# Kernel optimization log

Measured on AMD Instinct MI355X. Metric: run time of the kernel, lower is better.

The kernel has to match this reference:

```python
import jax, jax.numpy as jnp
import numpy as np

TWO_PI = 2.0 * np.pi
OMEGA = 1.0  # frequency scale from init


def setup_inputs() -> dict:
    key = jax.random.key(0)
    ks = jax.random.split(key, 10)
    B, G, D = 2, 32, 3
    C_IN, C, C_OUT, F, L = 4, 128, 2, 128, 4  # in/model/out channels, freqs, n_spectral_convs
    a = jax.random.normal(ks[0], (B, G, G, G, C_IN), dtype=jnp.float32)
    x = jax.random.uniform(ks[1], (B, G, G, G, D), dtype=jnp.float32)
    y = jax.random.uniform(ks[2], (B, G, G, G, D), dtype=jnp.float32)
    fc_in_w = jax.random.normal(ks[3], (C_IN, C), dtype=jnp.float32) / np.sqrt(C_IN)
    fc_in_b = jnp.zeros((C,), dtype=jnp.float32)
    freqs = jax.random.normal(ks[4], (L, F, D), dtype=jnp.float32)  # per-layer spatial frequencies
    w_real = jax.random.normal(ks[5], (L, C, C, F), dtype=jnp.float32) * 0.05
    w_imag = jax.random.normal(ks[6], (L, C, C, F), dtype=jnp.float32) * 0.05
    fc_out_w = jax.random.normal(ks[7], (C, C_OUT), dtype=jnp.float32) / np.sqrt(C)
    fc_out_b = jnp.zeros((C_OUT,), dtype=jnp.float32)
    return {"a": a, "x": x, "y": y, "fc_in_w": fc_in_w, "fc_in_b": fc_in_b,
            "freqs": freqs, "w_real": w_real, "w_imag": w_imag,
            "fc_out_w": fc_out_w, "fc_out_b": fc_out_b}


def _spectral_conv(hf, xin, xout, k, Wc):
    # hf: (B, N, C) real; xin/xout: (B, N, D); k: (F, D); Wc: (C, C, F) complex
    N = hf.shape[1]
    ang_in = TWO_PI * OMEGA * jnp.einsum('bnd,fd->bnf', xin, k)
    phi_in = jnp.exp(-1j * ang_in.astype(jnp.complex64))          # (B, N, F)
    H = jnp.einsum('bnc,bnf->bcf', hf.astype(jnp.complex64), phi_in) / N  # forward transform
    G = jnp.einsum('bcf,cof->bof', H, Wc)                          # per-frequency channel mixing
    ang_out = TWO_PI * OMEGA * jnp.einsum('bnd,fd->bnf', xout, k)
    phi_out = jnp.exp(1j * ang_out.astype(jnp.complex64))          # (B, N, F)
    return jnp.real(jnp.einsum('bof,bnf->bno', G, phi_out))       # inverse evaluation at xout


def reference(a, x, y, fc_in_w, fc_in_b, freqs, w_real, w_imag, fc_out_w, fc_out_b):
    B = a.shape[0]
    spatial = a.shape[1:4]
    hf = jnp.einsum('...i,io->...o', a, fc_in_w) + fc_in_b
    hf = hf.reshape(B, -1, hf.shape[-1])               # (B, N, C)
    xf = x.reshape(B, -1, x.shape[-1])                 # (B, N, D)
    yf = y.reshape(B, -1, y.shape[-1])
    L = freqs.shape[0]
    for l in range(L):
        Wc = (w_real[l] + 1j * w_imag[l]).astype(jnp.complex64)
        pts_out = xf if l < L - 1 else yf              # last conv queries at y
        hf = jax.nn.gelu(_spectral_conv(hf, xf, pts_out, freqs[l], Wc))
    u = jnp.einsum('bnc,co->bno', hf, fc_out_w) + fc_out_b
    return u.reshape(B, *spatial, fc_out_w.shape[-1])
```

## Files before the change

kernel.cpp:

```cpp
#include <hip/hip_runtime.h>
#include <math.h>

#define Bb 2
#define Nn 32768
#define Cc 128
#define Ff 128
#define LL 4
#define SKN 128
#define PS 16448

typedef __attribute__((ext_vector_type(8))) short short8;
typedef __attribute__((ext_vector_type(4))) float float4v;
typedef __attribute__((ext_vector_type(2))) unsigned int uint2v;
typedef unsigned short ushort_t;
typedef unsigned int uint_t;

union frag_cast { short8 s; uint_t u[4]; };
union vec8 { float4v v[2]; float s[8]; };

__device__ inline uint_t asu(float f) { union { float f; uint_t u; } x; x.f = f; return x.u; }
__device__ inline float asf(uint_t u) { union { uint_t u; float f; } x; x.u = u; return x.f; }
__device__ inline uint_t pack_hi(float v0, float v1) {
    return __builtin_amdgcn_perm(asu(v1), asu(v0), 0x07060302u);
}
__device__ inline float resid(float v) { return v - asf(asu(v) & 0xffff0000u); }

typedef __attribute__((address_space(1))) const uint_t guint;
typedef __attribute__((address_space(3))) uint_t luint;
__device__ inline void gload16(const uint_t* g, uint_t* l) {
    __builtin_amdgcn_global_load_lds((guint*)g, (luint*)l, 16, 0, 0);
}

#define LBAR() asm volatile("s_waitcnt lgkmcnt(0)\n\ts_barrier" ::: "memory")
#define CBAR() asm volatile("s_waitcnt vmcnt(6) lgkmcnt(0)\n\ts_barrier" ::: "memory")

__global__ __launch_bounds__(256) void prep_xt(const float* __restrict__ x,
                                               const float* __restrict__ y,
                                               float* __restrict__ xT,
                                               float* __restrict__ yT) {
    int i = blockIdx.x * 256 + threadIdx.x;
    int b = i >> 15, n = i & 32767;
    const float* xp = x + (size_t)i * 3;
    const float* yp = y + (size_t)i * 3;
    size_t base = ((size_t)(b * 3) << 15) + n;
    xT[base] = xp[0]; xT[base + (1 << 15)] = xp[1]; xT[base + (2 << 15)] = xp[2];
    yT[base] = yp[0]; yT[base + (1 << 15)] = yp[1]; yT[base + (2 << 15)] = yp[2];
}

__global__ __launch_bounds__(256) void in_proj(const float* __restrict__ a,
                                               const float* __restrict__ w,
                                               const float* __restrict__ bias,
                                               uint_t* __restrict__ hfTh,
                                               uint_t* __restrict__ hfTl) {
    int idx = blockIdx.x * 256 + threadIdx.x;
    int np = idx & 16383;
    int c = (idx >> 14) & 127;
    int b = idx >> 21;
    int n = np * 2;
    const float* ap = a + (((size_t)(b << 15)) + n) * 4;
    float s0 = bias[c], s1 = s0;
#pragma unroll
    for (int i = 0; i < 4; ++i) { s0 += ap[i] * w[i * Cc + c]; s1 += ap[4 + i] * w[i * Cc + c]; }
    hfTh[idx] = pack_hi(s0, s1);
    hfTl[idx] = pack_hi(resid(s0), resid(s1));
}

__global__ __launch_bounds__(512, 2) void fwd_lds(const uint_t* __restrict__ hfTh,
                                                  const uint_t* __restrict__ hfTl,
                                                  const float* __restrict__ xT,
                                                  const float* __restrict__ freqs,
                                                  float* __restrict__ Spart) {
    __shared__ __align__(16) uint_t Ah_s[2][2048], Al_s[2][2048];

    const int sk = blockIdx.x;
    const int b = blockIdx.y;
    const int tid = threadIdx.x, lane = tid & 63, wave = tid >> 6;
    const int h = wave & 1, wn = wave >> 1;
    const int fr = lane & 15, kg = lane >> 4;

    float kx[2], ky[2], kz[2];
#pragma unroll
    for (int ni = 0; ni < 2; ++ni) {
        int f = wn * 32 + ni * 16 + fr;
        kx[ni] = freqs[f * 3 + 0];
        ky[ni] = freqs[f * 3 + 1];
        kz[ni] = freqs[f * 3 + 2];
    }

    const float* xb = xT + ((size_t)(b * 3) << 15);
    const int srow = wave * 16 + (lane >> 2);
    const size_t gbase = ((size_t)(b * 128 + srow) << 14) + (size_t)((lane & 3) * 4);
    const int npair0 = sk * 128;

    float4v acc[8][2];
#pragma unroll
    for (int mi = 0; mi < 8; ++mi)
#pragma unroll
        for (int ni = 0; ni < 2; ++ni) acc[mi][ni] = (float4v){0.f, 0.f, 0.f, 0.f};

    vec8 X0[2], X1[2], X2[2];
    gload16(hfTh + gbase + npair0, &Ah_s[0][wave * 256]);
    gload16(hfTl + gbase + npair0, &Al_s[0][wave * 256]);
    __builtin_amdgcn_sched_barrier(0);
    {
        const int nbase = sk * 256 + kg * 8;
        X0[0].v[0] = *(const float4v*)(xb + nbase);
        X0[0].v[1] = *(const float4v*)(xb + nbase + 4);
        X1[0].v[0] = *(const float4v*)(xb + (1 << 15) + nbase);
        X1[0].v[1] = *(const float4v*)(xb + (1 << 15) + nbase + 4);
        X2[0].v[0] = *(const float4v*)(xb + (2 << 15) + nbase);
        X2[0].v[1] = *(const float4v*)(xb + (2 << 15) + nbase + 4);
    }

#pragma unroll
    for (int kt = 0; kt < 8; ++kt) {
        const int cur = kt & 1, nxt = cur ^ 1;
        CBAR();
        if (kt < 7) {
            gload16(hfTh + gbase + npair0 + (kt + 1) * 16, &Ah_s[nxt][wave * 256]);
            gload16(hfTl + gbase + npair0 + (kt + 1) * 16, &Al_s[nxt][wave * 256]);
            __builtin_amdgcn_sched_barrier(0);
            const int nbase2 = sk * 256 + (kt + 1) * 32 + kg * 8;
            X0[nxt].v[0] = *(const float4v*)(xb + nbase2);
            X0[nxt].v[1] = *(const float4v*)(xb + nbase2 + 4);
            X1[nxt].v[0] = *(const float4v*)(xb + (1 << 15) + nbase2);
            X1[nxt].v[1] = *(const float4v*)(xb + (1 << 15) + nbase2 + 4);
            X2[nxt].v[0] = *(const float4v*)(xb + (2 << 15) + nbase2);
            X2[nxt].v[1] = *(const float4v*)(xb + (2 << 15) + nbase2 + 4);
        }
        float r[16], tv[16];
#pragma unroll
        for (int ni = 0; ni < 2; ++ni)
#pragma unroll
            for (int q = 0; q < 4; ++q) {
                float rv0 = X0[cur].s[2 * q] * kx[ni] + X1[cur].s[2 * q] * ky[ni] + X2[cur].s[2 * q] * kz[ni];
                float rv1 = X0[cur].s[2 * q + 1] * kx[ni] + X1[cur].s[2 * q + 1] * ky[ni] + X2[cur].s[2 * q + 1] * kz[ni];
                r[ni * 8 + 2 * q] = __builtin_amdgcn_fractf(rv0);
                r[ni * 8 + 2 * q + 1] = __builtin_amdgcn_fractf(rv1);
            }
        if (h) {
#pragma unroll
            for (int i = 0; i < 16; ++i) tv[i] = __builtin_amdgcn_sinf(r[i]);
        } else {
#pragma unroll
            for (int i = 0; i < 16; ++i) tv[i] = __builtin_amdgcn_cosf(r[i]);
        }
        frag_cast bhf[2], blf[2];
#pragma unroll
        for (int ni = 0; ni < 2; ++ni)
#pragma unroll
            for (int q = 0; q < 4; ++q) {
                float v0 = tv[ni * 8 + 2 * q], v1 = tv[ni * 8 + 2 * q + 1];
                bhf[ni].u[q] = pack_hi(v0, v1);
                blf[ni].u[q] = pack_hi(resid(v0), resid(v1));
            }
#pragma unroll
        for (int mi = 0; mi < 8; ++mi) {
            frag_cast ah, al;
            ah.s = *(const short8*)&Ah_s[cur][(mi * 16 + fr) * 16 + kg * 4];
            al.s = *(const short8*)&Al_s[cur][(mi * 16 + fr) * 16 + kg * 4];
#pragma unroll
            for (int ni = 0; ni < 2; ++ni) {
                acc[mi][ni] = __builtin_amdgcn_mfma_f32_16x16x32_bf16(ah.s, bhf[ni].s, acc[mi][ni], 0, 0, 0);
                acc[mi][ni] = __builtin_amdgcn_mfma_f32_16x16x32_bf16(ah.s, blf[ni].s, acc[mi][ni], 0, 0, 0);
                acc[mi][ni] = __builtin_amdgcn_mfma_f32_16x16x32_bf16(al.s, bhf[ni].s, acc[mi][ni], 0, 0, 0);
            }
        }
    }

    float* op = Spart + (size_t)((b * 2 + h) * SKN + sk) * PS;
#pragma unroll
    for (int mi = 0; mi < 8; ++mi)
#pragma unroll
        for (int ni = 0; ni < 2; ++ni)
#pragma unroll
            for (int r2 = 0; r2 < 4; ++r2) {
                int c = mi * 16 + kg * 4 + r2;
                int f = wn * 32 + ni * 16 + fr;
                op[c * 128 + f] = acc[mi][ni][r2];
            }
}

__global__ __launch_bounds__(512, 2) void inv_fwd(const uint_t* __restrict__ Gh,
                                                  const uint_t* __restrict__ Gl,
                                                  const float* __restrict__ xT,
                                                  const float* __restrict__ fI,
                                                  const float* __restrict__ fF,
                                                  float* __restrict__ Spart) {
    __shared__ float kxs[128], kys[128], kzs[128];
    __shared__ __align__(16) float Xs[3][256];
    __shared__ __align__(16) uint_t Ah_s[4096], Al_s[4096];
    __shared__ __align__(16) uint_t Hh_s[2560], Hl_s[2560];
    const int chunk = blockIdx.x, b = blockIdx.y;
    const int tid = threadIdx.x, lane = tid & 63, wn = tid >> 6;
    const int fr = lane & 15, kg = lane >> 4;
    const int h = wn & 1, wf = wn >> 1;
    const int n0 = chunk * 256;

    if (tid < 128) {
        kxs[tid] = fI[tid * 3 + 0];
        kys[tid] = fI[tid * 3 + 1];
        kzs[tid] = fI[tid * 3 + 2];
    }
    for (int i = tid; i < 768; i += 512) {
        int d = i >> 8, nn = i & 255;
        Xs[d][nn] = xT[((size_t)(b * 3 + d) << 15) + n0 + nn];
    }

    frag_cast bh[8], bl[8];
#pragma unroll
    for (int kt = 0; kt < 8; ++kt) {
        size_t gi = ((size_t)(b * 128 + wn * 16 + fr)) * 128 + kt * 16 + kg * 4;
        bh[kt].s = *(const short8*)(Gh + gi);
        bl[kt].s = *(const short8*)(Gl + gi);
    }

    float kxf[2], kyf[2], kzf[2];
#pragma unroll
    for (int ni = 0; ni < 2; ++ni) {
        int f = wf * 32 + ni * 16 + fr;
        kxf[ni] = fF[f * 3 + 0];
        kyf[ni] = fF[f * 3 + 1];
        kzf[ni] = fF[f * 3 + 2];
    }

    float4v accF[8][2];
#pragma unroll
    for (int mi = 0; mi < 8; ++mi)
#pragma unroll
        for (int ni = 0; ni < 2; ++ni) accF[mi][ni] = (float4v){0.f, 0.f, 0.f, 0.f};

    __syncthreads();

    for (int p = 0; p < 8; ++p) {
        const int nsub = p * 32;

        {
            const int kt = wn;
            float4v kxv = *(const float4v*)&kxs[kt * 16 + kg * 4];
            float4v kyv = *(const float4v*)&kys[kt * 16 + kg * 4];
            float4v kzv = *(const float4v*)&kzs[kt * 16 + kg * 4];
#pragma unroll
            for (int mi2 = 0; mi2 < 2; ++mi2) {
                float px = Xs[0][nsub + mi2 * 16 + fr];
                float py = Xs[1][nsub + mi2 * 16 + fr];
                float pz = Xs[2][nsub + mi2 * 16 + fr];
                frag_cast ah, al;
#pragma unroll
                for (int q = 0; q < 4; ++q) {
                    float rev = px * kxv[q] + py * kyv[q] + pz * kzv[q];
                    float rr = __builtin_amdgcn_fractf(rev);
                    float cv = __builtin_amdgcn_cosf(rr);
                    float sv = __builtin_amdgcn_sinf(rr);
                    ah.u[q] = pack_hi(cv, sv);
                    al.u[q] = pack_hi(resid(cv), resid(sv));
                }
                *(short8*)&Ah_s[((mi2 * 8 + kt) * 64 + lane) * 4] = ah.s;
                *(short8*)&Al_s[((mi2 * 8 + kt) * 64 + lane) * 4] = al.s;
            }
        }
        LBAR();

        {
            float4v ahh[2], ahl[2], alh[2];
#pragma unroll
            for (int mi2 = 0; mi2 < 2; ++mi2) {
                ahh[mi2] = (float4v){0.f, 0.f, 0.f, 0.f};
                ahl[mi2] = (float4v){0.f, 0.f, 0.f, 0.f};
                alh[mi2] = (float4v){0.f, 0.f, 0.f, 0.f};
            }
#pragma unroll
            for (int kt = 0; kt < 8; ++kt) {
#pragma unroll
                for (int mi2 = 0; mi2 < 2; ++mi2) {
                    frag_cast ah, al;
                    ah.s = *(const short8*)&Ah_s[((mi2 * 8 + kt) * 64 + lane) * 4];
                    al.s = *(const short8*)&Al_s[((mi2 * 8 + kt) * 64 + lane) * 4];
                    ahh[mi2] = __builtin_amdgcn_mfma_f32_16x16x32_bf16(ah.s, bh[kt].s, ahh[mi2], 0, 0, 0);
                    ahl[mi2] = __builtin_amdgcn_mfma_f32_16x16x32_bf16(ah.s, bl[kt].s, ahl[mi2], 0, 0, 0);
                    alh[mi2] = __builtin_amdgcn_mfma_f32_16x16x32_bf16(al.s, bh[kt].s, alh[mi2], 0, 0, 0);
                }
            }
#pragma unroll
            for (int mi2 = 0; mi2 < 2; ++mi2) {
                float g[4];
#pragma unroll
                for (int r2 = 0; r2 < 4; ++r2) {
                    float v = ahh[mi2][r2] + (ahl[mi2][r2] + alh[mi2][r2]);
                    float u2 = 1.5957691216057308f * (v + 0.044715f * v * v * v);
                    float t = 1.0f - 2.0f / (1.0f + __expf(u2));
                    g[r2] = 0.5f * v * (1.0f + t);
                }
                int row = wn * 16 + fr;
                uint2v hv = { pack_hi(g[0], g[1]), pack_hi(g[2], g[3]) };
                uint2v lv = { pack_hi(resid(g[0]), resid(g[1])), pack_hi(resid(g[2]), resid(g[3])) };
                *(uint2v*)&Hh_s[row * 20 + mi2 * 8 + kg * 2] = hv;
                *(uint2v*)&Hl_s[row * 20 + mi2 * 8 + kg * 2] = lv;
            }
        }
        LBAR();

        {
            vec8 x0, x1, x2;
            x0.v[0] = *(const float4v*)&Xs[0][nsub + kg * 8];
            x0.v[1] = *(const float4v*)&Xs[0][nsub + kg * 8 + 4];
            x1.v[0] = *(const float4v*)&Xs[1][nsub + kg * 8];
            x1.v[1] = *(const float4v*)&Xs[1][nsub + kg * 8 + 4];
            x2.v[0] = *(const float4v*)&Xs[2][nsub + kg * 8];
            x2.v[1] = *(const float4v*)&Xs[2][nsub + kg * 8 + 4];
            float r[16], tv[16];
#pragma unroll
            for (int ni = 0; ni < 2; ++ni)
#pragma unroll
                for (int q = 0; q < 4; ++q) {
                    float rv0 = x0.s[2 * q] * kxf[ni] + x1.s[2 * q] * kyf[ni] + x2.s[2 * q] * kzf[ni];
                    float rv1 = x0.s[2 * q + 1] * kxf[ni] + x1.s[2 * q + 1] * kyf[ni] + x2.s[2 * q + 1] * kzf[ni];
                    r[ni * 8 + 2 * q] = __builtin_amdgcn_fractf(rv0);
                    r[ni * 8 + 2 * q + 1] = __builtin_amdgcn_fractf(rv1);
                }
            if (h) {
#pragma unroll
                for (int i = 0; i < 16; ++i) tv[i] = __builtin_amdgcn_sinf(r[i]);
            } else {
#pragma unroll
                for (int i = 0; i < 16; ++i) tv[i] = __builtin_amdgcn_cosf(r[i]);
            }
            frag_cast bhf[2], blf[2];
#pragma unroll
            for (int ni = 0; ni < 2; ++ni)
#pragma unroll
                for (int q = 0; q < 4; ++q) {
                    float v0 = tv[ni * 8 + 2 * q], v1 = tv[ni * 8 + 2 * q + 1];
                    bhf[ni].u[q] = pack_hi(v0, v1);
                    blf[ni].u[q] = pack_hi(resid(v0), resid(v1));
                }
#pragma unroll
            for (int mi = 0; mi < 8; ++mi) {
                frag_cast ah, al;
                ah.s = *(const short8*)&Hh_s[(mi * 16 + fr) * 20 + kg * 4];
                al.s = *(const short8*)&Hl_s[(mi * 16 + fr) * 20 + kg * 4];
#pragma unroll
                for (int ni = 0; ni < 2; ++ni) {
                    accF[mi][ni] = __builtin_amdgcn_mfma_f32_16x16x32_bf16(ah.s, bhf[ni].s, accF[mi][ni], 0, 0, 0);
                    accF[mi][ni] = __builtin_amdgcn_mfma_f32_16x16x32_bf16(ah.s, blf[ni].s, accF[mi][ni], 0, 0, 0);
                    accF[mi][ni] = __builtin_amdgcn_mfma_f32_16x16x32_bf16(al.s, bhf[ni].s, accF[mi][ni], 0, 0, 0);
                }
            }
        }
        LBAR();
    }

    float* op = Spart + (size_t)((b * 2 + h) * SKN + chunk) * PS;
#pragma unroll
    for (int mi = 0; mi < 8; ++mi)
#pragma unroll
        for (int ni = 0; ni < 2; ++ni)
#pragma unroll
            for (int r2 = 0; r2 < 4; ++r2) {
                int c = mi * 16 + kg * 4 + r2;
                int f = wf * 32 + ni * 16 + fr;
                op[c * 128 + f] = accF[mi][ni][r2];
            }
}

__global__ __launch_bounds__(256) void reduce_kernel(const float* __restrict__ Spart,
                                                     float* __restrict__ S) {
    __shared__ float red[4][64];
    const int chunk = blockIdx.x, bh = blockIdx.y;
    const int tid = threadIdx.x;
    const int cfl = tid & 63, q = tid >> 6;
    const float* p = Spart + (size_t)bh * SKN * PS + (size_t)(q * 32) * PS + chunk * 64 + cfl;
    float s = 0.0f;
#pragma unroll 8
    for (int k = 0; k < 32; ++k) s += p[(size_t)k * PS];
    red[q][cfl] = s;
    __syncthreads();
    if (tid < 64) {
        float t = red[0][tid] + red[1][tid] + red[2][tid] + red[3][tid];
        S[bh * 16384 + chunk * 64 + tid] = t;
    }
}

__global__ __launch_bounds__(256) void mix_kernel(const float* __restrict__ S,
                                                  const float* __restrict__ Wre,
                                                  const float* __restrict__ Wim,
                                                  uint_t* __restrict__ Gh,
                                                  uint_t* __restrict__ Gl) {
    __shared__ float Stile[4][128][16];
    const int ot = blockIdx.x;
    const int ft = blockIdx.y;
    const int tid = threadIdx.x;
    const int fl = tid & 15, ol = (tid >> 4) & 1, cg = tid >> 5;
    const int o = ot * 2 + ol, f0 = ft * 16;

    for (int i = tid; i < 8192; i += 256) {
        int bh = i >> 11, c = (i >> 4) & 127, ff = i & 15;
        Stile[bh][c][ff] = S[(size_t)bh * 16384 + c * 128 + f0 + ff];
    }
    __syncthreads();

    float g0 = 0.f, g1 = 0.f, g2 = 0.f, g3 = 0.f;
#pragma unroll 4
    for (int c = cg * 16; c < cg * 16 + 16; ++c) {
        float wr = Wre[((size_t)(c * 128 + o)) * 128 + f0 + fl];
        float wi = Wim[((size_t)(c * 128 + o)) * 128 + f0 + fl];
        float sc0 = Stile[0][c][fl], ss0 = Stile[1][c][fl];
        float sc1 = Stile[2][c][fl], ss1 = Stile[3][c][fl];
        g0 += sc0 * wr + ss0 * wi;  g1 += ss0 * wr - sc0 * wi;
        g2 += sc1 * wr + ss1 * wi;  g3 += ss1 * wr - sc1 * wi;
    }
    __syncthreads();
    float4v* rp = (float4v*)Stile;
    rp[cg * 32 + ol * 16 + fl] = (float4v){g0, g1, g2, g3};
    __syncthreads();
    if (tid < 32) {
        int tol = tid >> 4, tfl = tid & 15;
        float4v r = rp[tid];
#pragma unroll
        for (int j = 1; j < 8; ++j) r += rp[j * 32 + tid];
        const float invN = 1.0f / (float)Nn;
        float gre0 = r[0] * invN, gmi0 = r[1] * invN;
        float gre1 = r[2] * invN, gmi1 = r[3] * invN;
        int oo = ot * 2 + tol;
        Gh[(0 * 128 + oo) * 128 + f0 + tfl] = pack_hi(gre0, gmi0);
        Gl[(0 * 128 + oo) * 128 + f0 + tfl] = pack_hi(resid(gre0), resid(gmi0));
        Gh[(1 * 128 + oo) * 128 + f0 + tfl] = pack_hi(gre1, gmi1);
        Gl[(1 * 128 + oo) * 128 + f0 + tfl] = pack_hi(resid(gre1), resid(gmi1));
    }
}

template <int LAST>
__global__ __launch_bounds__(512, 4) void inv_reg(const uint_t* __restrict__ Gh,
                                                  const uint_t* __restrict__ Gl,
                                                  const float* __restrict__ ptsT,
                                                  const float* __restrict__ freqs,
                                                  uint_t* __restrict__ hfTh,
                                                  uint_t* __restrict__ hfTl,
                                                  const float* __restrict__ ow,
                                                  const float* __restrict__ ob,
                                                  float* __restrict__ u) {
    __shared__ __align__(16) float kxs[128], kys[128], kzs[128];
    __shared__ __align__(16) uint_t Ah_s[4096];
    __shared__ __align__(16) uint_t Al_s[4096];
    __shared__ float redo[8][32][2];
    const int nt = blockIdx.x, b = blockIdx.y;
    const int tid = threadIdx.x, lane = tid & 63, wn = tid >> 6;
    const int fr = lane & 15, kg = lane >> 4;

    if (tid < 128) {
        kxs[tid] = freqs[tid * 3 + 0];
        kys[tid] = freqs[tid * 3 + 1];
        kzs[tid] = freqs[tid * 3 + 2];
    }

    frag_cast bh[8], bl[8];
#pragma unroll
    for (int kt = 0; kt < 8; ++kt) {
        size_t gi = ((size_t)(b * 128 + wn * 16 + fr)) * 128 + kt * 16 + kg * 4;
        bh[kt].s = *(const short8*)(Gh + gi);
        bl[kt].s = *(const short8*)(Gl + gi);
    }

    float w0v = 0.f, w1v = 0.f;
    if (LAST) {
        int o = wn * 16 + fr;
        w0v = ow[o * 2 + 0];
        w1v = ow[o * 2 + 1];
    }

    const float* pb = ptsT + ((size_t)(b * 3) << 15);
    const int n0 = nt * 64;

    float px[4], py[4], pz[4];
#pragma unroll
    for (int m = 0; m < 4; ++m) {
        int n = n0 + m * 16 + fr;
        px[m] = pb[n]; py[m] = pb[(1 << 15) + n]; pz[m] = pb[(2 << 15) + n];
    }

    __syncthreads();

#pragma unroll
    for (int ph = 0; ph < 2; ++ph) {
        {
            const int kt = wn;
            float4v kxv = *(const float4v*)&kxs[kt * 16 + kg * 4];
            float4v kyv = *(const float4v*)&kys[kt * 16 + kg * 4];
            float4v kzv = *(const float4v*)&kzs[kt * 16 + kg * 4];
#pragma unroll
            for (int mi2 = 0; mi2 < 2; ++mi2) {
                const int m = ph * 2 + mi2;
                frag_cast ah, al;
#pragma unroll
                for (int q = 0; q < 4; ++q) {
                    float rev = px[m] * kxv[q] + py[m] * kyv[q] + pz[m] * kzv[q];
                    float rr = __builtin_amdgcn_fractf(rev);
                    float cv = __builtin_amdgcn_cosf(rr);
                    float sv = __builtin_amdgcn_sinf(rr);
                    ah.u[q] = pack_hi(cv, sv);
                    al.u[q] = pack_hi(resid(cv), resid(sv));
                }
                *(short8*)&Ah_s[((mi2 * 8 + kt) * 64 + lane) * 4] = ah.s;
                *(short8*)&Al_s[((mi2 * 8 + kt) * 64 + lane) * 4] = al.s;
            }
        }
        LBAR();

        float4v ahh[2], ahl[2], alh[2];
#pragma unroll
        for (int mi2 = 0; mi2 < 2; ++mi2) {
            ahh[mi2] = (float4v){0.f, 0.f, 0.f, 0.f};
            ahl[mi2] = (float4v){0.f, 0.f, 0.f, 0.f};
            alh[mi2] = (float4v){0.f, 0.f, 0.f, 0.f};
        }
#pragma unroll
        for (int kt = 0; kt < 8; ++kt) {
#pragma unroll
            for (int mi2 = 0; mi2 < 2; ++mi2) {
                frag_cast ah, al;
                ah.s = *(const short8*)&Ah_s[((mi2 * 8 + kt) * 64 + lane) * 4];
                al.s = *(const short8*)&Al_s[((mi2 * 8 + kt) * 64 + lane) * 4];
                ahh[mi2] = __builtin_amdgcn_mfma_f32_16x16x32_bf16(ah.s, bh[kt].s, ahh[mi2], 0, 0, 0);
                ahl[mi2] = __builtin_amdgcn_mfma_f32_16x16x32_bf16(ah.s, bl[kt].s, ahl[mi2], 0, 0, 0);
                alh[mi2] = __builtin_amdgcn_mfma_f32_16x16x32_bf16(al.s, bh[kt].s, alh[mi2], 0, 0, 0);
            }
        }
        LBAR();

        float ps[2][2][4];
        if (LAST) {
#pragma unroll
            for (int mi2 = 0; mi2 < 2; ++mi2)
#pragma unroll
                for (int j = 0; j < 2; ++j)
#pragma unroll
                    for (int r2 = 0; r2 < 4; ++r2) ps[mi2][j][r2] = 0.f;
        }
#pragma unroll
        for (int mi2 = 0; mi2 < 2; ++mi2) {
            const int m = ph * 2 + mi2;
            float g[4];
#pragma unroll
            for (int r2 = 0; r2 < 4; ++r2) {
                float v = ahh[mi2][r2] + (ahl[mi2][r2] + alh[mi2][r2]);
                float u2 = 1.5957691216057308f * (v + 0.044715f * v * v * v);
                float t = 1.0f - 2.0f / (1.0f + __expf(u2));
                g[r2] = 0.5f * v * (1.0f + t);
            }
            if (!LAST) {
                int o = wn * 16 + fr;
                int nb = n0 + m * 16 + kg * 4;
                size_t di = ((size_t)(b * 128 + o) << 14) + (nb >> 1);
                uint2v hv = { pack_hi(g[0], g[1]), pack_hi(g[2], g[3]) };
                uint2v lv = { pack_hi(resid(g[0]), resid(g[1])), pack_hi(resid(g[2]), resid(g[3])) };
                *(uint2v*)(hfTh + di) = hv;
                *(uint2v*)(hfTl + di) = lv;
            } else {
#pragma unroll
                for (int r2 = 0; r2 < 4; ++r2) {
                    ps[mi2][0][r2] += g[r2] * w0v;
                    ps[mi2][1][r2] += g[r2] * w1v;
                }
            }
        }

        if (LAST) {
#pragma unroll
            for (int mi2 = 0; mi2 < 2; ++mi2)
#pragma unroll
                for (int j = 0; j < 2; ++j)
#pragma unroll
                    for (int r2 = 0; r2 < 4; ++r2) {
                        float v = ps[mi2][j][r2];
                        v += __shfl_xor(v, 1);
                        v += __shfl_xor(v, 2);
                        v += __shfl_xor(v, 4);
                        v += __shfl_xor(v, 8);
                        ps[mi2][j][r2] = v;
                    }
            if (fr == 0) {
#pragma unroll
                for (int mi2 = 0; mi2 < 2; ++mi2)
#pragma unroll
                    for (int r2 = 0; r2 < 4; ++r2) {
                        redo[wn][mi2 * 16 + kg * 4 + r2][0] = ps[mi2][0][r2];
                        redo[wn][mi2 * 16 + kg * 4 + r2][1] = ps[mi2][1][r2];
                    }
            }
            LBAR();
            if (tid < 64) {
                int nl = tid >> 1, j = tid & 1;
                float val = ob[j];
#pragma unroll
                for (int w8 = 0; w8 < 8; ++w8) val += redo[w8][nl][j];
                u[((size_t)((b << 15) + n0 + ph * 32 + nl)) * 2 + j] = val;
            }
            LBAR();
        }
    }
}

extern "C" void kernel_launch(void* const* d_in, const int* in_sizes, int n_in,
                              void* d_out, int out_size, void* d_ws, size_t ws_size,
                              hipStream_t stream) {
    const float* a        = (const float*)d_in[0];
    const float* x        = (const float*)d_in[1];
    const float* y        = (const float*)d_in[2];
    const float* fc_in_w  = (const float*)d_in[3];
    const float* fc_in_b  = (const float*)d_in[4];
    const float* freqs    = (const float*)d_in[5];
    const float* w_real   = (const float*)d_in[6];
    const float* w_imag   = (const float*)d_in[7];
    const float* fc_out_w = (const float*)d_in[8];
    const float* fc_out_b = (const float*)d_in[9];
    float* out = (float*)d_out;

    uint_t* ws    = (uint_t*)d_ws;
    uint_t* hfTh  = ws;
    uint_t* hfTl  = hfTh + (size_t)Bb * Cc * Nn / 2;
    float*  Spart = (float*)(hfTl + (size_t)Bb * Cc * Nn / 2);
    float*  S     = Spart + (size_t)Bb * 2 * SKN * PS;
    uint_t* Gh    = (uint_t*)(S + (size_t)Bb * 2 * Cc * Ff);
    uint_t* Gl    = Gh + (size_t)Bb * Cc * Ff;
    float*  xT    = (float*)(Gl + (size_t)Bb * Cc * Ff);
    float*  yT    = xT + (size_t)Bb * 3 * Nn;

    prep_xt<<<(Bb * Nn) / 256, 256, 0, stream>>>(x, y, xT, yT);
    in_proj<<<(Bb * Cc * Nn / 2) / 256, 256, 0, stream>>>(a, fc_in_w, fc_in_b, hfTh, hfTl);

    fwd_lds<<<dim3(SKN, Bb), 512, 0, stream>>>(hfTh, hfTl, xT, freqs, Spart);
    reduce_kernel<<<dim3(256, 4), 256, 0, stream>>>(Spart, S);
    mix_kernel<<<dim3(64, 8), 256, 0, stream>>>(S, w_real, w_imag, Gh, Gl);

    for (int l = 0; l < LL - 1; ++l) {
        const float* kI  = freqs  + (size_t)l * Ff * 3;
        const float* kF  = freqs  + (size_t)(l + 1) * Ff * 3;
        const float* Wre = w_real + (size_t)(l + 1) * Cc * Cc * Ff;
        const float* Wim = w_imag + (size_t)(l + 1) * Cc * Cc * Ff;

        inv_fwd<<<dim3(128, Bb), 512, 0, stream>>>(Gh, Gl, xT, kI, kF, Spart);
        reduce_kernel<<<dim3(256, 4), 256, 0, stream>>>(Spart, S);
        mix_kernel<<<dim3(64, 8), 256, 0, stream>>>(S, Wre, Wim, Gh, Gl);
    }

    inv_reg<1><<<dim3(512, Bb), 512, 0, stream>>>(Gh, Gl, yT, freqs + (size_t)(LL - 1) * Ff * 3,
                                                  hfTh, hfTl, fc_out_w, fc_out_b, out);
}
```

Baseline: 330.7 us.

## Split inv_fwd work across 16 waves per block instead of 8

```diff
diff --git a/kernel.cpp b/kernel.cpp
--- a/kernel.cpp
+++ b/kernel.cpp
@@ -181,20 +181,21 @@
             }
 }
 
-__global__ __launch_bounds__(512, 2) void inv_fwd(const uint_t* __restrict__ Gh,
-                                                  const uint_t* __restrict__ Gl,
-                                                  const float* __restrict__ xT,
-                                                  const float* __restrict__ fI,
-                                                  const float* __restrict__ fF,
-                                                  float* __restrict__ Spart) {
+__global__ __launch_bounds__(1024, 4) void inv_fwd(const uint_t* __restrict__ Gh,
+                                                   const uint_t* __restrict__ Gl,
+                                                   const float* __restrict__ xT,
+                                                   const float* __restrict__ fI,
+                                                   const float* __restrict__ fF,
+                                                   float* __restrict__ Spart) {
     __shared__ float kxs[128], kys[128], kzs[128];
     __shared__ __align__(16) float Xs[3][256];
     __shared__ __align__(16) uint_t Ah_s[4096], Al_s[4096];
     __shared__ __align__(16) uint_t Hh_s[2560], Hl_s[2560];
     const int chunk = blockIdx.x, b = blockIdx.y;
-    const int tid = threadIdx.x, lane = tid & 63, wn = tid >> 6;
+    const int tid = threadIdx.x, lane = tid & 63, wv = tid >> 6;
     const int fr = lane & 15, kg = lane >> 4;
-    const int h = wn & 1, wf = wn >> 1;
+    const int og = wv & 7, mh = wv >> 3;
+    const int h = wv & 1, wf = (wv >> 1) & 3, fh = wv >> 3;
     const int n0 = chunk * 256;
 
     if (tid < 128) {
@@ -202,15 +203,15 @@
         kys[tid] = fI[tid * 3 + 1];
         kzs[tid] = fI[tid * 3 + 2];
     }
-    for (int i = tid; i < 768; i += 512) {
-        int d = i >> 8, nn = i & 255;
+    if (tid < 768) {
+        int d = tid >> 8, nn = tid & 255;
         Xs[d][nn] = xT[((size_t)(b * 3 + d) << 15) + n0 + nn];
     }
 
     frag_cast bh[8], bl[8];
 #pragma unroll
     for (int kt = 0; kt < 8; ++kt) {
-        size_t gi = ((size_t)(b * 128 + wn * 16 + fr)) * 128 + kt * 16 + kg * 4;
+        size_t gi = ((size_t)(b * 128 + og * 16 + fr)) * 128 + kt * 16 + kg * 4;
         bh[kt].s = *(const short8*)(Gh + gi);
         bl[kt].s = *(const short8*)(Gl + gi);
     }
@@ -224,11 +225,11 @@
         kzf[ni] = fF[f * 3 + 2];
     }
 
-    float4v accF[8][2];
-#pragma unroll
-    for (int mi = 0; mi < 8; ++mi)
-#pragma unroll
-        for (int ni = 0; ni < 2; ++ni) accF[mi][ni] = (float4v){0.f, 0.f, 0.f, 0.f};
+    float4v accF[4][2];
+#pragma unroll
+    for (int mi4 = 0; mi4 < 4; ++mi4)
+#pragma unroll
+        for (int ni = 0; ni < 2; ++ni) accF[mi4][ni] = (float4v){0.f, 0.f, 0.f, 0.f};
 
     __syncthreads();
 
@@ -236,67 +237,54 @@
         const int nsub = p * 32;
 
         {
-            const int kt = wn;
+            const int kt = og;
             float4v kxv = *(const float4v*)&kxs[kt * 16 + kg * 4];
             float4v kyv = *(const float4v*)&kys[kt * 16 + kg * 4];
             float4v kzv = *(const float4v*)&kzs[kt * 16 + kg * 4];
-#pragma unroll
-            for (int mi2 = 0; mi2 < 2; ++mi2) {
-                float px = Xs[0][nsub + mi2 * 16 + fr];
-                float py = Xs[1][nsub + mi2 * 16 + fr];
-                float pz = Xs[2][nsub + mi2 * 16 + fr];
+            float px = Xs[0][nsub + mh * 16 + fr];
+            float py = Xs[1][nsub + mh * 16 + fr];
+            float pz = Xs[2][nsub + mh * 16 + fr];
+            frag_cast ah, al;
+#pragma unroll
+            for (int q = 0; q < 4; ++q) {
+                float rev = px * kxv[q] + py * kyv[q] + pz * kzv[q];
+                float rr = __builtin_amdgcn_fractf(rev);
+                float cv = __builtin_amdgcn_cosf(rr);
+                float sv = __builtin_amdgcn_sinf(rr);
+                ah.u[q] = pack_hi(cv, sv);
+                al.u[q] = pack_hi(resid(cv), resid(sv));
+            }
+            *(short8*)&Ah_s[((mh * 8 + kt) * 64 + lane) * 4] = ah.s;
+            *(short8*)&Al_s[((mh * 8 + kt) * 64 + lane) * 4] = al.s;
+        }
+        LBAR();
+
+        {
+            float4v ahh = (float4v){0.f, 0.f, 0.f, 0.f};
+            float4v ahl = (float4v){0.f, 0.f, 0.f, 0.f};
+            float4v alh = (float4v){0.f, 0.f, 0.f, 0.f};
+#pragma unroll
+            for (int kt = 0; kt < 8; ++kt) {
                 frag_cast ah, al;
-#pragma unroll
-                for (int q = 0; q < 4; ++q) {
-                    float rev = px * kxv[q] + py * kyv[q] + pz * kzv[q];
-                    float rr = __builtin_amdgcn_fractf(rev);
-                    float cv = __builtin_amdgcn_cosf(rr);
-                    float sv = __builtin_amdgcn_sinf(rr);
-                    ah.u[q] = pack_hi(cv, sv);
-                    al.u[q] = pack_hi(resid(cv), resid(sv));
-                }
-                *(short8*)&Ah_s[((mi2 * 8 + kt) * 64 + lane) * 4] = ah.s;
-                *(short8*)&Al_s[((mi2 * 8 + kt) * 64 + lane) * 4] = al.s;
-            }
-        }
-        LBAR();
-
-        {
-            float4v ahh[2], ahl[2], alh[2];
-#pragma unroll
-            for (int mi2 = 0; mi2 < 2; ++mi2) {
-                ahh[mi2] = (float4v){0.f, 0.f, 0.f, 0.f};
-                ahl[mi2] = (float4v){0.f, 0.f, 0.f, 0.f};
-                alh[mi2] = (float4v){0.f, 0.f, 0.f, 0.f};
-            }
-#pragma unroll
-            for (int kt = 0; kt < 8; ++kt) {
-#pragma unroll
-                for (int mi2 = 0; mi2 < 2; ++mi2) {
-                    frag_cast ah, al;
-                    ah.s = *(const short8*)&Ah_s[((mi2 * 8 + kt) * 64 + lane) * 4];
-                    al.s = *(const short8*)&Al_s[((mi2 * 8 + kt) * 64 + lane) * 4];
-                    ahh[mi2] = __builtin_amdgcn_mfma_f32_16x16x32_bf16(ah.s, bh[kt].s, ahh[mi2], 0, 0, 0);
-                    ahl[mi2] = __builtin_amdgcn_mfma_f32_16x16x32_bf16(ah.s, bl[kt].s, ahl[mi2], 0, 0, 0);
-                    alh[mi2] = __builtin_amdgcn_mfma_f32_16x16x32_bf16(al.s, bh[kt].s, alh[mi2], 0, 0, 0);
-                }
-            }
-#pragma unroll
-            for (int mi2 = 0; mi2 < 2; ++mi2) {
-                float g[4];
-#pragma unroll
-                for (int r2 = 0; r2 < 4; ++r2) {
-                    float v = ahh[mi2][r2] + (ahl[mi2][r2] + alh[mi2][r2]);
-                    float u2 = 1.5957691216057308f * (v + 0.044715f * v * v * v);
-                    float t = 1.0f - 2.0f / (1.0f + __expf(u2));
-                    g[r2] = 0.5f * v * (1.0f + t);
-                }
-                int row = wn * 16 + fr;
-                uint2v hv = { pack_hi(g[0], g[1]), pack_hi(g[2], g[3]) };
-                uint2v lv = { pack_hi(resid(g[0]), resid(g[1])), pack_hi(resid(g[2]), resid(g[3])) };
-                *(uint2v*)&Hh_s[row * 20 + mi2 * 8 + kg * 2] = hv;
-                *(uint2v*)&Hl_s[row * 20 + mi2 * 8 + kg * 2] = lv;
-            }
+                ah.s = *(const short8*)&Ah_s[((mh * 8 + kt) * 64 + lane) * 4];
+                al.s = *(const short8*)&Al_s[((mh * 8 + kt) * 64 + lane) * 4];
+                ahh = __builtin_amdgcn_mfma_f32_16x16x32_bf16(ah.s, bh[kt].s, ahh, 0, 0, 0);
+                ahl = __builtin_amdgcn_mfma_f32_16x16x32_bf16(ah.s, bl[kt].s, ahl, 0, 0, 0);
+                alh = __builtin_amdgcn_mfma_f32_16x16x32_bf16(al.s, bh[kt].s, alh, 0, 0, 0);
+            }
+            float g[4];
+#pragma unroll
+            for (int r2 = 0; r2 < 4; ++r2) {
+                float v = ahh[r2] + (ahl[r2] + alh[r2]);
+                float u2 = 1.5957691216057308f * (v + 0.044715f * v * v * v);
+                float t = 1.0f - 2.0f / (1.0f + __expf(u2));
+                g[r2] = 0.5f * v * (1.0f + t);
+            }
+            int row = og * 16 + fr;
+            uint2v hv = { pack_hi(g[0], g[1]), pack_hi(g[2], g[3]) };
+            uint2v lv = { pack_hi(resid(g[0]), resid(g[1])), pack_hi(resid(g[2]), resid(g[3])) };
+            *(uint2v*)&Hh_s[row * 20 + mh * 8 + kg * 2] = hv;
+            *(uint2v*)&Hl_s[row * 20 + mh * 8 + kg * 2] = lv;
         }
         LBAR();
 
@@ -335,15 +323,16 @@
                     blf[ni].u[q] = pack_hi(resid(v0), resid(v1));
                 }
 #pragma unroll
-            for (int mi = 0; mi < 8; ++mi) {
+            for (int mi4 = 0; mi4 < 4; ++mi4) {
+                const int mi = fh * 4 + mi4;
                 frag_cast ah, al;
                 ah.s = *(const short8*)&Hh_s[(mi * 16 + fr) * 20 + kg * 4];
                 al.s = *(const short8*)&Hl_s[(mi * 16 + fr) * 20 + kg * 4];
 #pragma unroll
                 for (int ni = 0; ni < 2; ++ni) {
-                    accF[mi][ni] = __builtin_amdgcn_mfma_f32_16x16x32_bf16(ah.s, bhf[ni].s, accF[mi][ni], 0, 0, 0);
-                    accF[mi][ni] = __builtin_amdgcn_mfma_f32_16x16x32_bf16(ah.s, blf[ni].s, accF[mi][ni], 0, 0, 0);
-                    accF[mi][ni] = __builtin_amdgcn_mfma_f32_16x16x32_bf16(al.s, bhf[ni].s, accF[mi][ni], 0, 0, 0);
+                    accF[mi4][ni] = __builtin_amdgcn_mfma_f32_16x16x32_bf16(ah.s, bhf[ni].s, accF[mi4][ni], 0, 0, 0);
+                    accF[mi4][ni] = __builtin_amdgcn_mfma_f32_16x16x32_bf16(ah.s, blf[ni].s, accF[mi4][ni], 0, 0, 0);
+                    accF[mi4][ni] = __builtin_amdgcn_mfma_f32_16x16x32_bf16(al.s, bhf[ni].s, accF[mi4][ni], 0, 0, 0);
                 }
             }
         }
@@ -352,14 +341,14 @@
 
     float* op = Spart + (size_t)((b * 2 + h) * SKN + chunk) * PS;
 #pragma unroll
-    for (int mi = 0; mi < 8; ++mi)
+    for (int mi4 = 0; mi4 < 4; ++mi4)
 #pragma unroll
         for (int ni = 0; ni < 2; ++ni)
 #pragma unroll
             for (int r2 = 0; r2 < 4; ++r2) {
-                int c = mi * 16 + kg * 4 + r2;
+                int c = (fh * 4 + mi4) * 16 + kg * 4 + r2;
                 int f = wf * 32 + ni * 16 + fr;
-                op[c * 128 + f] = accF[mi][ni][r2];
+                op[c * 128 + f] = accF[mi4][ni][r2];
             }
 }
 
@@ -638,7 +627,7 @@
         const float* Wre = w_real + (size_t)(l + 1) * Cc * Cc * Ff;
         const float* Wim = w_imag + (size_t)(l + 1) * Cc * Cc * Ff;
 
-        inv_fwd<<<dim3(128, Bb), 512, 0, stream>>>(Gh, Gl, xT, kI, kF, Spart);
+        inv_fwd<<<dim3(128, Bb), 1024, 0, stream>>>(Gh, Gl, xT, kI, kF, Spart);
         reduce_kernel<<<dim3(256, 4), 256, 0, stream>>>(Spart, S);
         mix_kernel<<<dim3(64, 8), 256, 0, stream>>>(S, Wre, Wim, Gh, Gl);
     }
```

After: 417.2 us. +26.1%, slower.
